# Kernel optimization log

Measured on AMD Instinct MI355X. Metric: run time of the kernel, lower is better.

## Reference

```python
import jax, jax.numpy as jnp
import numpy as np

N = 50000          # nodes
E = 1600000        # edges (avg degree 32)
C_E = 64           # edge feature channels
C_N = 256          # node feature channels
C_OUT = 256        # output channels


def setup_inputs() -> dict:
    key = jax.random.key(0)
    ks = jax.random.split(key, 8)
    D = jax.random.uniform(ks[0], (N,), dtype=jnp.float32) + 0.5  # degree-like, bounded away from 0
    row_idx = jax.random.randint(ks[1], (E,), 0, N)               # destination node of each edge
    edge_attr = jax.random.normal(ks[2], (E, C_E), dtype=jnp.float32)
    X = jax.random.normal(ks[3], (N, C_N), dtype=jnp.float32)
    # learned params (nn.Linear: y = x @ W.T + b); store transposed for x @ W
    W_pass = jax.random.normal(ks[4], (C_E, C_OUT), dtype=jnp.float32) / np.sqrt(C_E)
    b_pass = jax.random.normal(ks[5], (C_OUT,), dtype=jnp.float32) * 0.01
    W_self = jax.random.normal(ks[6], (C_N, C_OUT), dtype=jnp.float32) / np.sqrt(C_N)
    b_self = jax.random.normal(ks[7], (C_OUT,), dtype=jnp.float32) * 0.01
    return {"D": D, "row_idx": row_idx, "edge_attr": edge_attr, "X": X,
            "W_pass": W_pass, "b_pass": b_pass, "W_self": W_self, "b_self": b_self}


def reference(D, row_idx, edge_attr, X, W_pass, b_pass, W_self, b_self):
    # torch.sparse.sum(A, dim=1).to_dense(): sum edge features into their row node -> (N, C_E)
    A = jax.ops.segment_sum(edge_attr, row_idx, num_segments=D.shape[0])
    # pass_map(A / D[:, None]) + self_map(X), then ReLU
    out = (A / D[:, None]) @ W_pass + b_pass + X @ W_self + b_self
    return jax.nn.relu(out)
```

## Files before the change

kernel.cpp:

```cpp
#include <hip/hip_runtime.h>
#include <hip/hip_bf16.h>

#define NNODES 50000
#define NEDGES 1600000
#define CE 64
#define CN 256
#define COUT 256
#define KTOT (CE + CN)
#define BCAP 64

typedef __attribute__((ext_vector_type(8))) short bf16x8;
typedef __attribute__((ext_vector_type(4))) float f32x4;

__device__ inline ushort f2bf(float f) {
    __hip_bfloat16 h = __float2bfloat16(f);
    return *(ushort*)&h;
}

__global__ __launch_bounds__(256) void fill_kernel(
    const int* __restrict__ row_idx,
    const float* __restrict__ ea,
    int* __restrict__ counts,
    int* __restrict__ buckets,
    float* __restrict__ Aovf)
{
    int e = blockIdx.x * 256 + threadIdx.x;
    int r = row_idx[e];
    int pos = atomicAdd(&counts[r], 1);
    if (pos < BCAP) {
        buckets[r * BCAP + pos] = e;
    } else {
        for (int c = 0; c < CE; ++c)
            atomicAdd(&Aovf[r * CE + c], ea[e * CE + c]);
    }
}

__global__ __launch_bounds__(256) void prep_kernel(
    const float* __restrict__ Wp, const float* __restrict__ Ws,
    const float* __restrict__ bp, const float* __restrict__ bs,
    ushort* __restrict__ Wt, float* __restrict__ bias)
{
    int k = blockIdx.x;
    int n = threadIdx.x;
    float v = (k < CE) ? Wp[k * COUT + n] : Ws[(k - CE) * COUT + n];
    Wt[n * KTOT + k] = f2bf(v);
    if (k == 0) bias[n] = bp[n] + bs[n];
}

__global__ __launch_bounds__(256) void gather_kernel(
    const float4* __restrict__ ea4,
    const int* __restrict__ counts,
    const int* __restrict__ buckets,
    const float* __restrict__ D,
    const float4* __restrict__ Aovf4,
    ushort* __restrict__ Abf)
{
    const int wave = threadIdx.x >> 6;
    const int lane = threadIdx.x & 63;
    const int n = blockIdx.x * 4 + wave;
    const int sub = lane >> 4;
    const int c4  = lane & 15;

    int deg = counts[n];
    if (deg > BCAP) deg = BCAP;

    float4 acc = make_float4(0.f, 0.f, 0.f, 0.f);
    const int* bkt = &buckets[n * BCAP];
    int i = 0;
    for (; i + 4 <= deg; i += 4) {
        int e = bkt[i + sub];
        float4 v = ea4[e * 16 + c4];
        acc.x += v.x; acc.y += v.y; acc.z += v.z; acc.w += v.w;
    }
    if (i + sub < deg) {
        int e = bkt[i + sub];
        float4 v = ea4[e * 16 + c4];
        acc.x += v.x; acc.y += v.y; acc.z += v.z; acc.w += v.w;
    }
    acc.x += __shfl_xor(acc.x, 16); acc.x += __shfl_xor(acc.x, 32);
    acc.y += __shfl_xor(acc.y, 16); acc.y += __shfl_xor(acc.y, 32);
    acc.z += __shfl_xor(acc.z, 16); acc.z += __shfl_xor(acc.z, 32);
    acc.w += __shfl_xor(acc.w, 16); acc.w += __shfl_xor(acc.w, 32);

    if (sub == 0) {
        float invd = 1.0f / D[n];
        float4 prev = Aovf4[n * 16 + c4];
        ushort4 o;
        o.x = f2bf((acc.x + prev.x) * invd);
        o.y = f2bf((acc.y + prev.y) * invd);
        o.z = f2bf((acc.z + prev.z) * invd);
        o.w = f2bf((acc.w + prev.w) * invd);
        *(ushort4*)&Abf[n * CE + c4 * 4] = o;
    }
}

#define GBM 128
#define GBN 128
#define GBK 32
#define APAD 8

__global__ __launch_bounds__(256) void mfma_gemm_kernel(
    const ushort* __restrict__ Abf,
    const float* __restrict__ X,
    const ushort* __restrict__ Wt,
    const float* __restrict__ bias,
    float* __restrict__ out)
{
    __shared__ ushort sA[GBM][GBK + APAD];
    __shared__ ushort sB[GBN][GBK + APAD];

    const int tid  = threadIdx.x;
    const int row0 = blockIdx.x * GBM;
    const int col0 = blockIdx.y * GBN;
    const int wave = tid >> 6;
    const int lane = tid & 63;
    const int m16  = lane & 15;
    const int kg   = lane >> 4;
    const int wr   = (wave >> 1) * 64;
    const int wc   = (wave & 1) * 64;

    const int sr = tid >> 1;
    const int sh = tid & 1;

    f32x4 acc[4][4];
    #pragma unroll
    for (int i = 0; i < 4; ++i)
        #pragma unroll
        for (int j = 0; j < 4; ++j)
            acc[i][j] = (f32x4){0.f, 0.f, 0.f, 0.f};

    for (int k0 = 0; k0 < KTOT; k0 += GBK) {
        {
            int gn = row0 + sr;
            uint4 v0 = {0,0,0,0}, v1 = {0,0,0,0};
            if (k0 < CE) {
                if (gn < NNODES) {
                    const uint4* src = (const uint4*)(Abf + gn * CE + k0 + sh * 16);
                    v0 = src[0]; v1 = src[1];
                }
            } else {
                if (gn < NNODES) {
                    const float4* xs = (const float4*)(X + (size_t)gn * CN + (k0 - CE) + sh * 16);
                    float4 a = xs[0], b = xs[1], c = xs[2], d = xs[3];
                    union { ushort us[8]; uint4 u; } p0, p1;
                    p0.us[0]=f2bf(a.x); p0.us[1]=f2bf(a.y); p0.us[2]=f2bf(a.z); p0.us[3]=f2bf(a.w);
                    p0.us[4]=f2bf(b.x); p0.us[5]=f2bf(b.y); p0.us[6]=f2bf(b.z); p0.us[7]=f2bf(b.w);
                    p1.us[0]=f2bf(c.x); p1.us[1]=f2bf(c.y); p1.us[2]=f2bf(c.z); p1.us[3]=f2bf(c.w);
                    p1.us[4]=f2bf(d.x); p1.us[5]=f2bf(d.y); p1.us[6]=f2bf(d.z); p1.us[7]=f2bf(d.w);
                    v0 = p0.u; v1 = p1.u;
                }
            }
            *(uint4*)&sA[sr][sh * 16]     = v0;
            *(uint4*)&sA[sr][sh * 16 + 8] = v1;
        }
        {
            const uint4* src = (const uint4*)(Wt + (size_t)(col0 + sr) * KTOT + k0 + sh * 16);
            *(uint4*)&sB[sr][sh * 16]     = src[0];
            *(uint4*)&sB[sr][sh * 16 + 8] = src[1];
        }
        __syncthreads();

        bf16x8 aF[4], bF[4];
        #pragma unroll
        for (int i = 0; i < 4; ++i)
            aF[i] = *(const bf16x8*)&sA[wr + i * 16 + m16][kg * 8];
        #pragma unroll
        for (int j = 0; j < 4; ++j)
            bF[j] = *(const bf16x8*)&sB[wc + j * 16 + m16][kg * 8];
        #pragma unroll
        for (int i = 0; i < 4; ++i)
            #pragma unroll
            for (int j = 0; j < 4; ++j)
                acc[i][j] = __builtin_amdgcn_mfma_f32_16x16x32_bf16(aF[i], bF[j], acc[i][j], 0, 0, 0);
        __syncthreads();
    }

    #pragma unroll
    for (int j = 0; j < 4; ++j) {
        int col = col0 + wc + j * 16 + m16;
        float bv = bias[col];
        #pragma unroll
        for (int i = 0; i < 4; ++i) {
            int rbase = row0 + wr + i * 16 + kg * 4;
            #pragma unroll
            for (int t = 0; t < 4; ++t) {
                int row = rbase + t;
                if (row < NNODES)
                    out[(size_t)row * COUT + col] = fmaxf(acc[i][j][t] + bv, 0.f);
            }
        }
    }
}

extern "C" void kernel_launch(void* const* d_in, const int* in_sizes, int n_in,
                              void* d_out, int out_size, void* d_ws, size_t ws_size,
                              hipStream_t stream) {
    const float* D         = (const float*)d_in[0];
    const int*   row_idx   = (const int*)  d_in[1];
    const float* edge_attr = (const float*)d_in[2];
    const float* X         = (const float*)d_in[3];
    const float* W_pass    = (const float*)d_in[4];
    const float* b_pass    = (const float*)d_in[5];
    const float* W_self    = (const float*)d_in[6];
    const float* b_self    = (const float*)d_in[7];
    float* out = (float*)d_out;

    char* ws = (char*)d_ws;
    size_t off = 0;
    float* Aovf   = (float*)(ws + off); off += (size_t)NNODES * CE * 4;
    int*   counts = (int*)  (ws + off); off += (size_t)NNODES * 4;
    int*   buckets= (int*)  (ws + off); off += (size_t)NNODES * BCAP * 4;
    ushort* Abf   = (ushort*)(ws + off); off += (size_t)NNODES * CE * 2;
    ushort* Wt    = (ushort*)(ws + off); off += (size_t)COUT * KTOT * 2;
    float* bias   = (float*)(ws + off); off += (size_t)COUT * 4;

    hipMemsetAsync(Aovf, 0, (size_t)NNODES * CE * sizeof(float), stream);
    hipMemsetAsync(counts, 0, (size_t)NNODES * sizeof(int), stream);

    fill_kernel<<<dim3(NEDGES / 256), dim3(256), 0, stream>>>(
        row_idx, edge_attr, counts, buckets, Aovf);

    prep_kernel<<<dim3(KTOT), dim3(256), 0, stream>>>(
        W_pass, W_self, b_pass, b_self, Wt, bias);

    gather_kernel<<<dim3(NNODES / 4), dim3(256), 0, stream>>>(
        (const float4*)edge_attr, counts, buckets, D, (const float4*)Aovf, Abf);

    dim3 grid((NNODES + GBM - 1) / GBM, COUT / GBN);
    mfma_gemm_kernel<<<grid, dim3(256), 0, stream>>>(
        Abf, X, Wt, bias, out);
}
```

Before: 784.0 us.

## Fuse edge gather into GEMM and widen tile to full output width

Merges the segment-sum gather and the MFMA GEMM into one kernel. Each block gathers and normalizes the edge sums for its 128 nodes straight into shared memory, then runs a 128x256 GEMM over the full output width. This drops the Abf intermediate round trip and a kernel launch, and reads X only once instead of once per column tile. It also loads bucket indices once per wave and broadcasts them with shuffles, and skips the overflow read when degree is under the bucket cap. The cost is fewer blocks, about 391, which means lower parallelism during the latency-bound gather phase, plus higher register pressure from 32 accumulators.

```diff
diff --git a/kernel.cpp b/kernel.cpp
--- a/kernel.cpp
+++ b/kernel.cpp
@@ -8,6 +8,11 @@
 #define COUT 256
 #define KTOT (CE + CN)
 #define BCAP 64
+
+#define FBM 128
+#define FBN 256
+#define FBK 32
+#define PAD 8
 
 typedef __attribute__((ext_vector_type(8))) short bf16x8;
 typedef __attribute__((ext_vector_type(4))) float f32x4;
@@ -47,144 +52,158 @@
     if (k == 0) bias[n] = bp[n] + bs[n];
 }
 
-__global__ __launch_bounds__(256) void gather_kernel(
+__global__ __launch_bounds__(256, 2) void fused_kernel(
     const float4* __restrict__ ea4,
     const int* __restrict__ counts,
     const int* __restrict__ buckets,
     const float* __restrict__ D,
     const float4* __restrict__ Aovf4,
-    ushort* __restrict__ Abf)
-{
-    const int wave = threadIdx.x >> 6;
-    const int lane = threadIdx.x & 63;
-    const int n = blockIdx.x * 4 + wave;
-    const int sub = lane >> 4;
-    const int c4  = lane & 15;
-
-    int deg = counts[n];
-    if (deg > BCAP) deg = BCAP;
-
-    float4 acc = make_float4(0.f, 0.f, 0.f, 0.f);
-    const int* bkt = &buckets[n * BCAP];
-    int i = 0;
-    for (; i + 4 <= deg; i += 4) {
-        int e = bkt[i + sub];
-        float4 v = ea4[e * 16 + c4];
-        acc.x += v.x; acc.y += v.y; acc.z += v.z; acc.w += v.w;
-    }
-    if (i + sub < deg) {
-        int e = bkt[i + sub];
-        float4 v = ea4[e * 16 + c4];
-        acc.x += v.x; acc.y += v.y; acc.z += v.z; acc.w += v.w;
-    }
-    acc.x += __shfl_xor(acc.x, 16); acc.x += __shfl_xor(acc.x, 32);
-    acc.y += __shfl_xor(acc.y, 16); acc.y += __shfl_xor(acc.y, 32);
-    acc.z += __shfl_xor(acc.z, 16); acc.z += __shfl_xor(acc.z, 32);
-    acc.w += __shfl_xor(acc.w, 16); acc.w += __shfl_xor(acc.w, 32);
-
-    if (sub == 0) {
-        float invd = 1.0f / D[n];
-        float4 prev = Aovf4[n * 16 + c4];
-        ushort4 o;
-        o.x = f2bf((acc.x + prev.x) * invd);
-        o.y = f2bf((acc.y + prev.y) * invd);
-        o.z = f2bf((acc.z + prev.z) * invd);
-        o.w = f2bf((acc.w + prev.w) * invd);
-        *(ushort4*)&Abf[n * CE + c4 * 4] = o;
-    }
-}
-
-#define GBM 128
-#define GBN 128
-#define GBK 32
-#define APAD 8
-
-__global__ __launch_bounds__(256) void mfma_gemm_kernel(
-    const ushort* __restrict__ Abf,
     const float* __restrict__ X,
     const ushort* __restrict__ Wt,
     const float* __restrict__ bias,
     float* __restrict__ out)
 {
-    __shared__ ushort sA[GBM][GBK + APAD];
-    __shared__ ushort sB[GBN][GBK + APAD];
+    __shared__ ushort sAg0[FBM][FBK + PAD];
+    __shared__ ushort sAg1[FBM][FBK + PAD];
+    __shared__ ushort sX [FBM][FBK + PAD];
+    __shared__ ushort sB [FBN][FBK + PAD];
 
     const int tid  = threadIdx.x;
-    const int row0 = blockIdx.x * GBM;
-    const int col0 = blockIdx.y * GBN;
     const int wave = tid >> 6;
     const int lane = tid & 63;
-    const int m16  = lane & 15;
-    const int kg   = lane >> 4;
-    const int wr   = (wave >> 1) * 64;
-    const int wc   = (wave & 1) * 64;
-
-    const int sr = tid >> 1;
-    const int sh = tid & 1;
-
-    f32x4 acc[4][4];
+    const int row0 = blockIdx.x * FBM;
+
+    {
+        const int sub = lane >> 4;
+        const int c4  = lane & 15;
+
+        const int nb  = row0 + wave * 32 + (lane & 31);
+        const int nbc = (nb < NNODES) ? nb : (NNODES - 1);
+        const int   cntv = counts[nbc];
+        const float dvv  = D[nbc];
+
+        for (int lm = 0; lm < 32; ++lm) {
+            const int m = wave * 32 + lm;
+            const int n = row0 + m;
+            const int cshf = __shfl(cntv, lm);
+            const int rawdeg = (n < NNODES) ? cshf : 0;
+            const int deg = (rawdeg < BCAP) ? rawdeg : BCAP;
+
+            float4 a0 = make_float4(0.f, 0.f, 0.f, 0.f);
+            float4 a1 = make_float4(0.f, 0.f, 0.f, 0.f);
+            int bktv = 0;
+            if (n < NNODES) bktv = buckets[(size_t)n * BCAP + lane];
+
+            int i = 0;
+            for (; i + 8 <= deg; i += 8) {
+                const int e0 = __shfl(bktv, i + sub);
+                const int e1 = __shfl(bktv, i + 4 + sub);
+                const float4 v0 = ea4[(size_t)e0 * 16 + c4];
+                const float4 v1 = ea4[(size_t)e1 * 16 + c4];
+                a0.x += v0.x; a0.y += v0.y; a0.z += v0.z; a0.w += v0.w;
+                a1.x += v1.x; a1.y += v1.y; a1.z += v1.z; a1.w += v1.w;
+            }
+            for (; i < deg; i += 4) {
+                const int e0 = __shfl(bktv, i + sub);
+                if (i + sub < deg) {
+                    const float4 v0 = ea4[(size_t)e0 * 16 + c4];
+                    a0.x += v0.x; a0.y += v0.y; a0.z += v0.z; a0.w += v0.w;
+                }
+            }
+
+            a0.x += a1.x; a0.y += a1.y; a0.z += a1.z; a0.w += a1.w;
+            a0.x += __shfl_xor(a0.x, 16); a0.x += __shfl_xor(a0.x, 32);
+            a0.y += __shfl_xor(a0.y, 16); a0.y += __shfl_xor(a0.y, 32);
+            a0.z += __shfl_xor(a0.z, 16); a0.z += __shfl_xor(a0.z, 32);
+            a0.w += __shfl_xor(a0.w, 16); a0.w += __shfl_xor(a0.w, 32);
+
+            const float dv = __shfl(dvv, lm);
+            if (sub == 0) {
+                const float invd = (n < NNODES) ? (1.0f / dv) : 0.f;
+                float4 prev = make_float4(0.f, 0.f, 0.f, 0.f);
+                if (n < NNODES && rawdeg > BCAP)
+                    prev = Aovf4[(size_t)n * 16 + c4];
+                ushort4 o;
+                o.x = f2bf((a0.x + prev.x) * invd);
+                o.y = f2bf((a0.y + prev.y) * invd);
+                o.z = f2bf((a0.z + prev.z) * invd);
+                o.w = f2bf((a0.w + prev.w) * invd);
+                ushort* dst = (c4 < 8) ? &sAg0[m][c4 * 4] : &sAg1[m][(c4 - 8) * 4];
+                *(ushort4*)dst = o;
+            }
+        }
+    }
+
+    const int m16 = lane & 15;
+    const int kg  = lane >> 4;
+    const int wr  = (wave >> 1) * 64;
+    const int wc  = (wave & 1) * 128;
+    const int sr  = tid >> 1;
+    const int sh  = tid & 1;
+    const int brr = tid >> 2;
+    const int bq  = tid & 3;
+
+    f32x4 acc[4][8];
     #pragma unroll
     for (int i = 0; i < 4; ++i)
         #pragma unroll
-        for (int j = 0; j < 4; ++j)
+        for (int j = 0; j < 8; ++j)
             acc[i][j] = (f32x4){0.f, 0.f, 0.f, 0.f};
 
-    for (int k0 = 0; k0 < KTOT; k0 += GBK) {
-        {
-            int gn = row0 + sr;
-            uint4 v0 = {0,0,0,0}, v1 = {0,0,0,0};
-            if (k0 < CE) {
-                if (gn < NNODES) {
-                    const uint4* src = (const uint4*)(Abf + gn * CE + k0 + sh * 16);
-                    v0 = src[0]; v1 = src[1];
-                }
-            } else {
-                if (gn < NNODES) {
-                    const float4* xs = (const float4*)(X + (size_t)gn * CN + (k0 - CE) + sh * 16);
-                    float4 a = xs[0], b = xs[1], c = xs[2], d = xs[3];
-                    union { ushort us[8]; uint4 u; } p0, p1;
-                    p0.us[0]=f2bf(a.x); p0.us[1]=f2bf(a.y); p0.us[2]=f2bf(a.z); p0.us[3]=f2bf(a.w);
-                    p0.us[4]=f2bf(b.x); p0.us[5]=f2bf(b.y); p0.us[6]=f2bf(b.z); p0.us[7]=f2bf(b.w);
-                    p1.us[0]=f2bf(c.x); p1.us[1]=f2bf(c.y); p1.us[2]=f2bf(c.z); p1.us[3]=f2bf(c.w);
-                    p1.us[4]=f2bf(d.x); p1.us[5]=f2bf(d.y); p1.us[6]=f2bf(d.z); p1.us[7]=f2bf(d.w);
-                    v0 = p0.u; v1 = p1.u;
-                }
-            }
-            *(uint4*)&sA[sr][sh * 16]     = v0;
-            *(uint4*)&sA[sr][sh * 16 + 8] = v1;
-        }
-        {
-            const uint4* src = (const uint4*)(Wt + (size_t)(col0 + sr) * KTOT + k0 + sh * 16);
-            *(uint4*)&sB[sr][sh * 16]     = src[0];
-            *(uint4*)&sB[sr][sh * 16 + 8] = src[1];
+    #pragma unroll
+    for (int ks = 0; ks < KTOT / FBK; ++ks) {
+        const int k0 = ks * FBK;
+
+        #pragma unroll
+        for (int p = 0; p < 4; ++p) {
+            const int r = brr + p * 64;
+            const uint4 v = *(const uint4*)(Wt + (size_t)r * KTOT + k0 + bq * 8);
+            *(uint4*)&sB[r][bq * 8] = v;
+        }
+
+        if (ks >= 2) {
+            const int gn = row0 + sr;
+            uint4 v0 = {0, 0, 0, 0}, v1 = {0, 0, 0, 0};
+            if (gn < NNODES) {
+                const float4* xs = (const float4*)(X + (size_t)gn * CN + (k0 - CE) + sh * 16);
+                const float4 a = xs[0], b = xs[1], c = xs[2], d = xs[3];
+                union { ushort us[8]; uint4 u; } p0, p1;
+                p0.us[0]=f2bf(a.x); p0.us[1]=f2bf(a.y); p0.us[2]=f2bf(a.z); p0.us[3]=f2bf(a.w);
+                p0.us[4]=f2bf(b.x); p0.us[5]=f2bf(b.y); p0.us[6]=f2bf(b.z); p0.us[7]=f2bf(b.w);
+                p1.us[0]=f2bf(c.x); p1.us[1]=f2bf(c.y); p1.us[2]=f2bf(c.z); p1.us[3]=f2bf(c.w);
+                p1.us[4]=f2bf(d.x); p1.us[5]=f2bf(d.y); p1.us[6]=f2bf(d.z); p1.us[7]=f2bf(d.w);
+                v0 = p0.u; v1 = p1.u;
+            }
+            *(uint4*)&sX[sr][sh * 16]     = v0;
+            *(uint4*)&sX[sr][sh * 16 + 8] = v1;
         }
         __syncthreads();
 
-        bf16x8 aF[4], bF[4];
+        const ushort (*sa)[FBK + PAD] = (ks == 0) ? sAg0 : (ks == 1) ? sAg1 : sX;
+        bf16x8 aF[4];
         #pragma unroll
         for (int i = 0; i < 4; ++i)
-            aF[i] = *(const bf16x8*)&sA[wr + i * 16 + m16][kg * 8];
-        #pragma unroll
-        for (int j = 0; j < 4; ++j)
-            bF[j] = *(const bf16x8*)&sB[wc + j * 16 + m16][kg * 8];
-        #pragma unroll
-        for (int i = 0; i < 4; ++i)
+            aF[i] = *(const bf16x8*)&sa[wr + i * 16 + m16][kg * 8];
+        #pragma unroll
+        for (int j = 0; j < 8; ++j) {
+            const bf16x8 bFj = *(const bf16x8*)&sB[wc + j * 16 + m16][kg * 8];
             #pragma unroll
-            for (int j = 0; j < 4; ++j)
-                acc[i][j] = __builtin_amdgcn_mfma_f32_16x16x32_bf16(aF[i], bF[j], acc[i][j], 0, 0, 0);
+            for (int i = 0; i < 4; ++i)
+                acc[i][j] = __builtin_amdgcn_mfma_f32_16x16x32_bf16(aF[i], bFj, acc[i][j], 0, 0, 0);
+        }
         __syncthreads();
     }
 
     #pragma unroll
-    for (int j = 0; j < 4; ++j) {
-        int col = col0 + wc + j * 16 + m16;
-        float bv = bias[col];
+    for (int j = 0; j < 8; ++j) {
+        const int col = wc + j * 16 + m16;
+        const float bv = bias[col];
         #pragma unroll
         for (int i = 0; i < 4; ++i) {
-            int rbase = row0 + wr + i * 16 + kg * 4;
+            const int rbase = row0 + wr + i * 16 + kg * 4;
             #pragma unroll
             for (int t = 0; t < 4; ++t) {
-                int row = rbase + t;
+                const int row = rbase + t;
                 if (row < NNODES)
                     out[(size_t)row * COUT + col] = fmaxf(acc[i][j][t] + bv, 0.f);
             }
@@ -210,7 +229,6 @@
     float* Aovf   = (float*)(ws + off); off += (size_t)NNODES * CE * 4;
     int*   counts = (int*)  (ws + off); off += (size_t)NNODES * 4;
     int*   buckets= (int*)  (ws + off); off += (size_t)NNODES * BCAP * 4;
-    ushort* Abf   = (ushort*)(ws + off); off += (size_t)NNODES * CE * 2;
     ushort* Wt    = (ushort*)(ws + off); off += (size_t)COUT * KTOT * 2;
     float* bias   = (float*)(ws + off); off += (size_t)COUT * 4;
 
@@ -223,10 +241,7 @@
     prep_kernel<<<dim3(KTOT), dim3(256), 0, stream>>>(
         W_pass, W_self, b_pass, b_self, Wt, bias);
 
-    gather_kernel<<<dim3(NNODES / 4), dim3(256), 0, stream>>>(
-        (const float4*)edge_attr, counts, buckets, D, (const float4*)Aovf, Abf);
-
-    dim3 grid((NNODES + GBM - 1) / GBM, COUT / GBN);
-    mfma_gemm_kernel<<<grid, dim3(256), 0, stream>>>(
-        Abf, X, Wt, bias, out);
-}
+    fused_kernel<<<dim3((NNODES + FBM - 1) / FBM), dim3(256), 0, stream>>>(
+        (const float4*)edge_attr, counts, buckets, D, (const float4*)Aovf,
+        X, Wt, bias, out);
+}
```

Result: slower. 801.6 us (+2.2%).
